# Performance work log

Measured on AMD Instinct MI355X. Metric: run time of the kernel, lower is better.

## Reference

```python
import jax, jax.numpy as jnp
import numpy as np

B, D, L, H = 8, 512, 2048, 8
DH = D // H
NEG = -1e30


def setup_inputs() -> dict:
    key = jax.random.key(0)
    k1, k2, k3, k4 = jax.random.split(key, 4)
    queries = jax.random.normal(k1, (B, D, L), dtype=jnp.float32)
    mask = jax.random.randint(k2, (B, L), 0, 2, dtype=jnp.int32)
    w_mem = jax.random.normal(k3, (2 * D, D), dtype=jnp.float32) * (1.0 / np.sqrt(D))
    w_q = jax.random.normal(k4, (D, D), dtype=jnp.float32) * (1.0 / np.sqrt(D))
    return {"queries": queries, "mask": mask, "w_mem": w_mem, "w_q": w_q}


def reference(queries, mask, w_mem, w_q):
    # 1x1 conv == pointwise GEMM over channel dim. queries: [B, D, L]
    memory = jnp.einsum('od,bdl->blo', w_mem, queries)  # [B, L, 2D]
    query = jnp.einsum('od,bdl->blo', w_q, queries)     # [B, L, D]

    def split_heads(x):  # [B, L, C] -> [B, H, L, C/H]
        b, l, c = x.shape
        return x.reshape(b, l, H, c // H).transpose(0, 2, 1, 3)

    k, v = memory[..., :D], memory[..., D:]
    Q = split_heads(query) * (DH ** -0.5)  # [B, H, L, DH]
    K = split_heads(k)
    V = split_heads(v)

    logits = jnp.einsum('bhqd,bhkd->bhqk', Q, K)  # [B, H, L, L]
    m = mask.astype(jnp.float32)[:, None, None, :]  # [B, 1, 1, L]
    logits = logits * m + (1.0 - m) * NEG
    weights = jax.nn.softmax(logits, axis=-1)
    x = jnp.einsum('bhqk,bhkd->bhqd', weights, V)  # [B, H, L, DH]
    # combine heads -> [B, L, D] -> transpose back to [B, D, L]
    out = x.transpose(0, 2, 1, 3).reshape(B, L, D).transpose(0, 2, 1)
    return out
```

## Files before the change

kernel.cpp:

```cpp
#include <hip/hip_runtime.h>
#include <hip/hip_bf16.h>

#define NB 8
#define ND 512
#define NL 2048
#define NH 8
#define NDH 64
#define VROWS 72

typedef __attribute__((ext_vector_type(8))) short bf16x8;
typedef __attribute__((ext_vector_type(4))) float f32x4;
typedef __attribute__((ext_vector_type(4))) unsigned int u32x4;

__device__ __forceinline__ unsigned short f2bf(float x) {
    return (unsigned short)((__float_as_uint(x) + 0x8000u) >> 16);
}

__device__ __forceinline__ float exp2_fast(float x) {
#if __has_builtin(__builtin_amdgcn_exp2f)
    return __builtin_amdgcn_exp2f(x);
#else
    return exp2f(x);
#endif
}

__device__ __forceinline__ unsigned int pack_bf16(float a, float b) {
#if __has_builtin(__builtin_amdgcn_cvt_pk_bf16_f32)
    auto r = __builtin_amdgcn_cvt_pk_bf16_f32(a, b);
    unsigned int u;
    __builtin_memcpy(&u, &r, 4);
    return u;
#else
    unsigned int ua = __float_as_uint(a) + 0x8000u;
    unsigned int ub = __float_as_uint(b) + 0x8000u;
    return __builtin_amdgcn_perm(ub, ua, 0x07060302u);
#endif
}

__device__ __forceinline__ int perm64(int k) {
    return (k & 32) | ((k & 12) << 1) | ((k & 16) >> 2) | (k & 3);
}

__device__ __forceinline__ void async16(void* lds, const void* g) {
    __builtin_amdgcn_global_load_lds(
        (const __attribute__((address_space(1))) unsigned int*)g,
        (__attribute__((address_space(3))) unsigned int*)lds, 16, 0, 0);
}

__global__ __launch_bounds__(256) void prep(
    const float* __restrict__ qin,
    const float* __restrict__ w_mem, const float* __restrict__ w_q,
    const int* __restrict__ maskp,
    unsigned short* __restrict__ Xt, unsigned short* __restrict__ Wc,
    unsigned short* __restrict__ Vt, unsigned short* __restrict__ Kh,
    int* __restrict__ cmap, int* __restrict__ ntile, int* __restrict__ nvalid)
{
    const int bid = blockIdx.x;
    const int t = threadIdx.x;
    if (bid < 2048) {
        __shared__ __align__(16) unsigned short T[64][72];
        const int l0 = (bid & 31) * 64, d0 = ((bid >> 5) & 7) * 64, b = bid >> 8;
        const float* X = qin + ((size_t)b * ND + d0) * NL + l0;
        #pragma unroll
        for (int i = 0; i < 4; ++i) {
            int e = t + i * 256;
            int d = e >> 4, l4 = (e & 15) * 4;
            float4 v = *(const float4*)(X + (size_t)d * NL + l4);
            T[l4 + 0][d] = f2bf(v.x);
            T[l4 + 1][d] = f2bf(v.y);
            T[l4 + 2][d] = f2bf(v.z);
            T[l4 + 3][d] = f2bf(v.w);
        }
        __syncthreads();
        #pragma unroll
        for (int i = 0; i < 2; ++i) {
            int e = t + i * 256;
            int row = e >> 3, c8 = (e & 7) * 8;
            *(bf16x8*)(Xt + ((size_t)b * NL + l0 + row) * ND + d0 + c8) =
                *(const bf16x8*)&T[row][c8];
        }
    } else if (bid < 2432) {
        int idx = ((bid - 2048) * 256 + t) * 8;
        int o = idx >> 9, k = idx & 511;
        const float* src;
        float sc;
        if (o < 1024) { src = w_mem + (size_t)o * ND + k; sc = 1.0f; }
        else          { src = w_q + (size_t)(o - 1024) * ND + k;
                        sc = 0.125f * 1.4426950408889634f; }
        float4 f0 = *(const float4*)src;
        float4 f1 = *(const float4*)(src + 4);
        ushort4 p0 = { f2bf(f0.x * sc), f2bf(f0.y * sc), f2bf(f0.z * sc), f2bf(f0.w * sc) };
        ushort4 p1 = { f2bf(f1.x * sc), f2bf(f1.y * sc), f2bf(f1.z * sc), f2bf(f1.w * sc) };
        *(ushort4*)(Wc + idx) = p0;
        *(ushort4*)(Wc + idx + 4) = p1;
    } else {
        __shared__ int wsum[4];
        const int sb = bid - 2432;
        const int b = sb >> 3, hh = sb & 7;
        const int lane = t & 63, wv = t >> 6;
        int4 ma = *(const int4*)&maskp[b * NL + t * 8];
        int4 mb = *(const int4*)&maskp[b * NL + t * 8 + 4];
        int m[8] = {ma.x, ma.y, ma.z, ma.w, mb.x, mb.y, mb.z, mb.w};
        int loc = 0;
        #pragma unroll
        for (int i = 0; i < 8; ++i) loc += m[i];
        int sc = loc;
        #pragma unroll
        for (int off = 1; off < 64; off <<= 1) {
            int v = __shfl_up(sc, off);
            if (lane >= off) sc += v;
        }
        if (lane == 63) wsum[wv] = sc;
        __syncthreads();
        int wbase = 0;
        #pragma unroll
        for (int i = 0; i < 4; ++i) if (i < wv) wbase += wsum[i];
        int j = wbase + sc - loc;
        if (hh == 0) {
            int jj = j;
            #pragma unroll
            for (int i = 0; i < 8; ++i) {
                cmap[b * NL + t * 8 + i] = m[i] ? jj : -1;
                jj += m[i];
            }
        }
        const int nb = wsum[0] + wsum[1] + wsum[2] + wsum[3];
        const int Nt = (nb + 63) & ~63;
        if (hh == 0 && t == 0) { ntile[b] = Nt >> 6; nvalid[b] = nb; }
        const int pad = Nt - nb;
        for (int e = t; e < pad * 64; e += 256) {
            int jj = nb + (e >> 6), dd = e & 63;
            int slot = (jj & ~63) | perm64(jj & 63);
            Vt[(((size_t)(b * NH + hh)) * VROWS + dd) * NL + slot] = 0;
            Kh[(((size_t)(b * NH + hh)) * NL + jj) * NDH + dd] = 0;
        }
    }
}

__global__ __launch_bounds__(256, 3) void proj_mfma(
    const unsigned short* __restrict__ Wc,
    const unsigned short* __restrict__ Xt,
    const int* __restrict__ cmap,
    unsigned short* __restrict__ Kh,
    unsigned short* __restrict__ Qh,
    unsigned short* __restrict__ Vt)
{
    __shared__ __align__(16) unsigned short As[128 * 64];
    __shared__ __align__(16) unsigned short Bs[128 * 64];

    const int b  = blockIdx.z;
    const int m0 = blockIdx.y * 128;
    const int n0 = blockIdx.x * 128;
    const int t  = threadIdx.x;
    const int w = t >> 6, lane = t & 63, quad = lane >> 4, lq = lane & 15;
    const int wo = (w >> 1) * 64, wl = (w & 1) * 64;
    const int lr = lane >> 3;
    const int cbsw = (lane & 7) ^ lr;
    const bool isV = (m0 >= 512) && (m0 < 1024);
    const f32x4 z4 = {0.f, 0.f, 0.f, 0.f};
    const int sw[2] = {(quad ^ (lq & 7)) * 8, ((4 + quad) ^ (lq & 7)) * 8};

    f32x4 acc[4][4];
    #pragma unroll
    for (int im = 0; im < 4; ++im)
        #pragma unroll
        for (int in = 0; in < 4; ++in) acc[im][in] = z4;

    if (!isV) {
        for (int k0 = 0; k0 < ND; k0 += 64) {
            __syncthreads();
            #pragma unroll 2
            for (int i = w; i < 32; i += 4) {
                if (i < 16) {
                    int R = i * 8;
                    async16(&As[R * 64],
                            Wc + (size_t)(m0 + R + lr) * ND + k0 + cbsw * 8);
                } else {
                    int R = (i - 16) * 8;
                    async16(&Bs[R * 64],
                            Xt + ((size_t)b * NL + n0 + R + lr) * ND + k0 + cbsw * 8);
                }
            }
            __syncthreads();
            #pragma unroll
            for (int ks = 0; ks < 2; ++ks) {
                bf16x8 af[4], bfr[4];
                #pragma unroll
                for (int im = 0; im < 4; ++im)
                    af[im] = *(const bf16x8*)&As[(wo + im * 16 + lq) * 64 + sw[ks]];
                #pragma unroll
                for (int in = 0; in < 4; ++in)
                    bfr[in] = *(const bf16x8*)&Bs[(wl + in * 16 + lq) * 64 + sw[ks]];
                #pragma unroll
                for (int im = 0; im < 4; ++im)
                    #pragma unroll
                    for (int in = 0; in < 4; ++in)
                        acc[im][in] = __builtin_amdgcn_mfma_f32_16x16x32_bf16(
                            af[im], bfr[in], acc[im][in], 0, 0, 0);
            }
        }
        if (m0 < 512) {
            int j[4];
            #pragma unroll
            for (int in = 0; in < 4; ++in)
                j[in] = cmap[b * NL + n0 + wl + in * 16 + lq];
            #pragma unroll
            for (int im = 0; im < 4; ++im) {
                int o  = (m0 + wo + im * 16 + quad * 4) & 511;
                int hh = o >> 6, dh = o & 63;
                #pragma unroll
                for (int in = 0; in < 4; ++in) {
                    if (j[in] >= 0) {
                        ushort4 pk = { f2bf(acc[im][in][0]), f2bf(acc[im][in][1]),
                                       f2bf(acc[im][in][2]), f2bf(acc[im][in][3]) };
                        *(ushort4*)&Kh[(((size_t)b * NH + hh) * NL + j[in]) * NDH + dh] = pk;
                    }
                }
            }
        } else {
            #pragma unroll
            for (int im = 0; im < 4; ++im) {
                int o  = (m0 + wo + im * 16 + quad * 4) & 511;
                int hh = o >> 6, dh = o & 63;
                #pragma unroll
                for (int in = 0; in < 4; ++in) {
                    int l = n0 + wl + in * 16 + lq;
                    ushort4 pk = { f2bf(acc[im][in][0]), f2bf(acc[im][in][1]),
                                   f2bf(acc[im][in][2]), f2bf(acc[im][in][3]) };
                    *(ushort4*)&Qh[(((size_t)b * NH + hh) * NL + l) * NDH + dh] = pk;
                }
            }
        }
    } else {
        for (int k0 = 0; k0 < ND; k0 += 64) {
            __syncthreads();
            #pragma unroll 2
            for (int i = w; i < 32; i += 4) {
                if (i < 16) {
                    int R = i * 8;
                    async16(&As[R * 64],
                            Wc + (size_t)(m0 + R + lr) * ND + k0 + cbsw * 8);
                } else {
                    int R = (i - 16) * 8;
                    async16(&Bs[R * 64],
                            Xt + ((size_t)b * NL + n0 + R + lr) * ND + k0 + cbsw * 8);
                }
            }
            __syncthreads();
            #pragma unroll
            for (int ks = 0; ks < 2; ++ks) {
                bf16x8 af[4], bfr[4];
                #pragma unroll
                for (int im = 0; im < 4; ++im)
                    af[im] = *(const bf16x8*)&As[(wo + im * 16 + lq) * 64 + sw[ks]];
                #pragma unroll
                for (int in = 0; in < 4; ++in)
                    bfr[in] = *(const bf16x8*)&Bs[(wl + in * 16 + lq) * 64 + sw[ks]];
                #pragma unroll
                for (int im = 0; im < 4; ++im)
                    #pragma unroll
                    for (int in = 0; in < 4; ++in)
                        acc[im][in] = __builtin_amdgcn_mfma_f32_16x16x32_bf16(
                            bfr[im], af[in], acc[im][in], 0, 0, 0);
            }
        }
        #pragma unroll
        for (int im = 0; im < 4; ++im) {
            int l4 = n0 + wl + im * 16 + quad * 4;
            int4 j4 = *(const int4*)&cmap[b * NL + l4];
            int jj[4] = {j4.x, j4.y, j4.z, j4.w};
            int slot[4];
            #pragma unroll
            for (int r = 0; r < 4; ++r)
                slot[r] = (jj[r] & ~63) | perm64(jj[r] & 63);
            #pragma unroll
            for (int in = 0; in < 4; ++in) {
                int o  = m0 - 512 + wo + in * 16 + lq;
                int hh = o >> 6, dd = o & 63;
                const size_t rowbase = (((size_t)(b * NH + hh)) * VROWS + dd) * NL;
                #pragma unroll
                for (int r = 0; r < 4; ++r)
                    if (jj[r] >= 0)
                        Vt[rowbase + slot[r]] = f2bf(acc[im][in][r]);
            }
        }
    }
}

__global__ __launch_bounds__(512, 4) void attn_mfma(
    const unsigned short* __restrict__ Qh,
    const unsigned short* __restrict__ Kh,
    const unsigned short* __restrict__ Vt,
    const int* __restrict__ ntilep,
    const int* __restrict__ nvalidp,
    float* __restrict__ out)
{
    __shared__ __align__(16) unsigned short Ks2[2][64 * 64];
    __shared__ __align__(16) unsigned short Vs2[2][64 * 64];

    const int id = blockIdx.x;
    const int h  = id & 7;
    const int b  = (id >> 3) & 7;
    const int q0 = (id >> 6) * 256;
    const int t = threadIdx.x;
    const int w = t >> 6;
    const int lane = t & 63, quad = lane >> 4, lq = lane & 15;
    const int lr = lane >> 3;
    const int cbsw = (lane & 7) ^ lr;
    const f32x4 z4 = {0.f, 0.f, 0.f, 0.f};

    const unsigned short* Qg = Qh + ((size_t)(b * NH + h)) * NL * NDH;
    const unsigned short* Kg = Kh + ((size_t)(b * NH + h)) * NL * NDH;
    const unsigned short* Vg = Vt + ((size_t)(b * NH + h)) * VROWS * NL;
    const int ntiles = ntilep[b];

    const int sw0 = (quad ^ (lq & 7)) * 8;
    const int sw1 = ((4 + quad) ^ (lq & 7)) * 8;

    const unsigned short* kgp = Kg + (size_t)(w * 8 + lr) * NDH + cbsw * 8;
    const unsigned short* vgp = Vg + (size_t)(w * 8 + lr) * NL + cbsw * 8;

    auto stage = [&](unsigned short* Kd, unsigned short* Vd, int kn) {
        async16(Kd + w * 512, kgp + (size_t)kn * NDH);
        async16(Vd + w * 512, vgp + kn);
    };

    stage(Ks2[0], Vs2[0], 0);

    bf16x8 qf[2][2];
    #pragma unroll
    for (int ni = 0; ni < 2; ++ni)
        #pragma unroll
        for (int ks = 0; ks < 2; ++ks)
            qf[ni][ks] = *(const bf16x8*)
                &Qg[(size_t)(q0 + w * 32 + ni * 16 + lq) * NDH + ks * 32 + quad * 8];

    f32x4 oacc[4][2];
    #pragma unroll
    for (int dm = 0; dm < 4; ++dm)
        #pragma unroll
        for (int ni = 0; ni < 2; ++ni) oacc[dm][ni] = z4;
    float ls[2] = {0.f, 0.f};

    auto body = [&](const unsigned short* KsB, const unsigned short* VsB,
                    unsigned short* KsN, unsigned short* VsN,
                    int kn, bool pf) {
        __syncthreads();
        if (pf) stage(KsN, VsN, kn);

        const unsigned short* kb0 = KsB + lq * 64 + sw0;
        const unsigned short* kb1 = KsB + lq * 64 + sw1;
        const unsigned short* vb0 = VsB + lq * 64 + sw0;
        const unsigned short* vb1 = VsB + lq * 64 + sw1;

        f32x4 sacc[4][2];
        #pragma unroll
        for (int mi = 0; mi < 4; ++mi) {
            bf16x8 kf = *(const bf16x8*)&kb0[mi * 1024];
            sacc[mi][0] = __builtin_amdgcn_mfma_f32_16x16x32_bf16(kf, qf[0][0], z4, 0, 0, 0);
            sacc[mi][1] = __builtin_amdgcn_mfma_f32_16x16x32_bf16(kf, qf[1][0], z4, 0, 0, 0);
        }
        #pragma unroll
        for (int mi = 0; mi < 4; ++mi) {
            bf16x8 kf = *(const bf16x8*)&kb1[mi * 1024];
            sacc[mi][0] = __builtin_amdgcn_mfma_f32_16x16x32_bf16(kf, qf[0][1], sacc[mi][0], 0, 0, 0);
            sacc[mi][1] = __builtin_amdgcn_mfma_f32_16x16x32_bf16(kf, qf[1][1], sacc[mi][1], 0, 0, 0);
        }

        #pragma unroll
        for (int ks = 0; ks < 2; ++ks) {
            u32x4 pfu[2];
            #pragma unroll
            for (int half = 0; half < 2; ++half) {
                const int mi = ks * 2 + half, jp = half * 2;
                #pragma unroll
                for (int ni = 0; ni < 2; ++ni) {
                    float e0 = exp2_fast(sacc[mi][ni][0]);
                    float e1 = exp2_fast(sacc[mi][ni][1]);
                    float e2 = exp2_fast(sacc[mi][ni][2]);
                    float e3 = exp2_fast(sacc[mi][ni][3]);
                    pfu[ni][jp + 0] = pack_bf16(e0, e1);
                    pfu[ni][jp + 1] = pack_bf16(e2, e3);
                }
            }
            const unsigned short* vb = ks ? vb1 : vb0;
            #pragma unroll
            for (int dm = 0; dm < 4; ++dm) {
                bf16x8 vf = *(const bf16x8*)&vb[dm * 1024];
                oacc[dm][0] = __builtin_amdgcn_mfma_f32_16x16x32_bf16(
                    vf, __builtin_bit_cast(bf16x8, pfu[0]), oacc[dm][0], 0, 0, 0);
                oacc[dm][1] = __builtin_amdgcn_mfma_f32_16x16x32_bf16(
                    vf, __builtin_bit_cast(bf16x8, pfu[1]), oacc[dm][1], 0, 0, 0);
            }
            #pragma unroll
            for (int ni = 0; ni < 2; ++ni)
                #pragma unroll
                for (int jw = 0; jw < 4; ++jw) {
                    unsigned int u = pfu[ni][jw];
                    ls[ni] += __uint_as_float(u << 16);
                    ls[ni] += __uint_as_float(u & 0xFFFF0000u);
                }
        }
    };

    int kt = 0;
    #pragma unroll 1
    for (; kt + 2 <= ntiles; kt += 2) {
        body(Ks2[0], Vs2[0], Ks2[1], Vs2[1], (kt + 1) * 64, true);
        body(Ks2[1], Vs2[1], Ks2[0], Vs2[0], (kt + 2) * 64, kt + 2 < ntiles);
    }
    if (kt < ntiles)
        body(Ks2[0], Vs2[0], Ks2[1], Vs2[1], 0, false);

    const float padc = (float)(ntiles * 64 - nvalidp[b]);
    float inv[2];
    #pragma unroll
    for (int ni = 0; ni < 2; ++ni) {
        float s = ls[ni];
        s += __shfl_xor(s, 16);
        s += __shfl_xor(s, 32);
        inv[ni] = 1.0f / (s - padc);
    }

    #pragma unroll
    for (int dm = 0; dm < 4; ++dm)
        #pragma unroll
        for (int ni = 0; ni < 2; ++ni)
            #pragma unroll
            for (int r = 0; r < 4; ++r) {
                int dh = dm * 16 + quad * 4 + r;
                int l  = q0 + w * 32 + ni * 16 + lq;
                out[((size_t)b * ND + h * NDH + dh) * NL + l] =
                    oacc[dm][ni][r] * inv[ni];
            }
}

extern "C" void kernel_launch(void* const* d_in, const int* in_sizes, int n_in,
                              void* d_out, int out_size, void* d_ws, size_t ws_size,
                              hipStream_t stream) {
    const float* queries = (const float*)d_in[0];
    const int*   maskp   = (const int*)d_in[1];
    const float* w_mem   = (const float*)d_in[2];
    const float* w_q     = (const float*)d_in[3];
    float* out = (float*)d_out;

    const size_t headElems  = (size_t)NB * NH * NL * NDH;
    const size_t vElems     = (size_t)NB * NH * VROWS * NL;
    unsigned short* Kh = (unsigned short*)d_ws;
    unsigned short* Vt = Kh + headElems;
    unsigned short* Qh = Vt + vElems;
    unsigned short* Wc = Qh + headElems;
    unsigned short* Xt = Wc + (size_t)1536 * ND;
    int* cmap   = (int*)(Xt + (size_t)NB * NL * ND);
    int* ntile  = cmap + NB * NL;
    int* nvalid = ntile + NB;

    prep<<<2496, 256, 0, stream>>>(queries, w_mem, w_q, maskp,
                                   Xt, Wc, Vt, Kh, cmap, ntile, nvalid);

    dim3 g1(NL / 128, 1536 / 128, NB);
    proj_mfma<<<g1, 256, 0, stream>>>(Wc, Xt, cmap, Kh, Qh, Vt);

    attn_mfma<<<512, 512, 0, stream>>>(Qh, Kh, Vt, ntile, nvalid, out);
}
```

Measured before the change: 174.7 us.

## Stage 128-key tiles per barrier and accumulate row sums in fp32

The attention loop now stages two 64-key K/V tiles per double-buffer step, which halves the number of __syncthreads barriers and async staging rounds per key. A small tail path handles an odd tile count. The softmax denominator is now accumulated directly from the fp32 exp values rather than by unpacking the bf16-packed probabilities, which removes the unpack work. The cost is double the LDS per block (64 KB versus 32 KB), which likely lowers the number of resident blocks per CU below the launch-bounds target of 4. The row sums also change slightly numerically.

```diff
diff --git a/kernel.cpp b/kernel.cpp
--- a/kernel.cpp
+++ b/kernel.cpp
@@ -295,8 +295,8 @@
     const int* __restrict__ nvalidp,
     float* __restrict__ out)
 {
-    __shared__ __align__(16) unsigned short Ks2[2][64 * 64];
-    __shared__ __align__(16) unsigned short Vs2[2][64 * 64];
+    __shared__ __align__(16) unsigned short Ks2[2][2 * 64 * 64];
+    __shared__ __align__(16) unsigned short Vs2[2][2 * 64 * 64];
 
     const int id = blockIdx.x;
     const int h  = id & 7;
@@ -320,12 +320,14 @@
     const unsigned short* kgp = Kg + (size_t)(w * 8 + lr) * NDH + cbsw * 8;
     const unsigned short* vgp = Vg + (size_t)(w * 8 + lr) * NL + cbsw * 8;
 
-    auto stage = [&](unsigned short* Kd, unsigned short* Vd, int kn) {
-        async16(Kd + w * 512, kgp + (size_t)kn * NDH);
-        async16(Vd + w * 512, vgp + kn);
+    auto stage128 = [&](unsigned short* Kd, unsigned short* Vd, int kn) {
+        async16(Kd + w * 512,        kgp + (size_t)kn * NDH);
+        async16(Kd + 4096 + w * 512, kgp + (size_t)(kn + 64) * NDH);
+        async16(Vd + w * 512,        vgp + kn);
+        async16(Vd + 4096 + w * 512, vgp + kn + 64);
     };
 
-    stage(Ks2[0], Vs2[0], 0);
+    stage128(Ks2[0], Vs2[0], 0);
 
     bf16x8 qf[2][2];
     #pragma unroll
@@ -342,12 +344,7 @@
         for (int ni = 0; ni < 2; ++ni) oacc[dm][ni] = z4;
     float ls[2] = {0.f, 0.f};
 
-    auto body = [&](const unsigned short* KsB, const unsigned short* VsB,
-                    unsigned short* KsN, unsigned short* VsN,
-                    int kn, bool pf) {
-        __syncthreads();
-        if (pf) stage(KsN, VsN, kn);
-
+    auto sub = [&](const unsigned short* KsB, const unsigned short* VsB) {
         const unsigned short* kb0 = KsB + lq * 64 + sw0;
         const unsigned short* kb1 = KsB + lq * 64 + sw1;
         const unsigned short* vb0 = VsB + lq * 64 + sw0;
@@ -379,6 +376,7 @@
                     float e1 = exp2_fast(sacc[mi][ni][1]);
                     float e2 = exp2_fast(sacc[mi][ni][2]);
                     float e3 = exp2_fast(sacc[mi][ni][3]);
+                    ls[ni] += (e0 + e1) + (e2 + e3);
                     pfu[ni][jp + 0] = pack_bf16(e0, e1);
                     pfu[ni][jp + 1] = pack_bf16(e2, e3);
                 }
@@ -392,25 +390,32 @@
                 oacc[dm][1] = __builtin_amdgcn_mfma_f32_16x16x32_bf16(
                     vf, __builtin_bit_cast(bf16x8, pfu[1]), oacc[dm][1], 0, 0, 0);
             }
-            #pragma unroll
-            for (int ni = 0; ni < 2; ++ni)
-                #pragma unroll
-                for (int jw = 0; jw < 4; ++jw) {
-                    unsigned int u = pfu[ni][jw];
-                    ls[ni] += __uint_as_float(u << 16);
-                    ls[ni] += __uint_as_float(u & 0xFFFF0000u);
-                }
         }
     };
 
-    int kt = 0;
+    const int npairs = ntiles >> 1, odd = ntiles & 1;
+    int p = 0;
     #pragma unroll 1
-    for (; kt + 2 <= ntiles; kt += 2) {
-        body(Ks2[0], Vs2[0], Ks2[1], Vs2[1], (kt + 1) * 64, true);
-        body(Ks2[1], Vs2[1], Ks2[0], Vs2[0], (kt + 2) * 64, kt + 2 < ntiles);
-    }
-    if (kt < ntiles)
-        body(Ks2[0], Vs2[0], Ks2[1], Vs2[1], 0, false);
+    for (; p + 1 < npairs; ++p) {
+        const int cb = p & 1;
+        __syncthreads();
+        stage128(Ks2[cb ^ 1], Vs2[cb ^ 1], (p + 1) * 128);
+        sub(Ks2[cb], Vs2[cb]);
+        sub(Ks2[cb] + 4096, Vs2[cb] + 4096);
+    }
+    if (npairs > 0) {
+        const int cb = p & 1;
+        __syncthreads();
+        if (odd) stage128(Ks2[cb ^ 1], Vs2[cb ^ 1], npairs * 128);
+        sub(Ks2[cb], Vs2[cb]);
+        sub(Ks2[cb] + 4096, Vs2[cb] + 4096);
+        ++p;
+    }
+    if (odd) {
+        const int cb = p & 1;
+        __syncthreads();
+        sub(Ks2[cb], Vs2[cb]);
+    }
 
     const float padc = (float)(ntiles * 64 - nvalidp[b]);
     float inv[2];
```

After: 171.6 us. About the same (-1.8%).
